# Performance work log

Hardware: AMD Instinct MI355X
Metric: run time of the kernel (lower is better)

The kernel has to match this reference:

```python
import jax, jax.numpy as jnp
import numpy as np
from jax import lax

B, DIM, H, W = 4, 256, 128, 128
KS, LOC, STRIDES_CFG, HEADS = 5, [2, 3], [1, 2], 8
C2 = DIM // 2
GK = HEADS * KS  # per-pixel dynamic kernel channels

def _kernel_map(ks, kstride, kloc):
    # replicates LSAMixer.generate_kernel_map_1d
    axes, strides, start = [0], [1], 1
    for loc, s in zip(kloc, kstride):
        for num in range(0, loc - start):
            axes.append(num * s + axes[-1] + strides[-1])
            strides.append(s)
        start = loc
    patch = (axes[-1] + strides[-1]) * 2 - 1
    full_axes = [-a for a in axes[:0:-1]] + axes
    full_strides = strides[:0:-1] + strides
    return full_axes, full_strides, patch

OFFS, STRDS, PATCH = _kernel_map(KS, STRIDES_CFG, LOC)
PAD = PATCH // 2

def _pw(x, w, b):
    # 1x1 conv as GEMM
    return jnp.einsum('bchw,oc->bohw', x, w) + b[None, :, None, None]

def _dw(x, w, b, ph, pw):
    # depthwise conv, torch OIHW layout with I=1
    y = lax.conv_general_dilated(x, w, (1, 1), [(ph, ph), (pw, pw)],
                                 feature_group_count=x.shape[1],
                                 dimension_numbers=('NCHW', 'OIHW', 'NCHW'))
    return y + b[None, :, None, None]

def _fsa(x, kern, groups, axis):
    # dynamic local attention: for each tap k (offset a, stride s) gather the
    # average of x over the s-wide strided window along `axis`, weight it by
    # the per-head dynamic kernel, and accumulate.
    Bx, Cx, Hx, Wx = x.shape
    gd = Cx // groups
    K = len(OFFS)
    L = x.shape[axis]
    padcfg = [(0, 0)] * 4
    padcfg[axis] = (PAD, PAD)
    xp = jnp.pad(x, padcfg)
    taps = []
    for a, s in zip(OFFS, STRDS):
        start = a if a >= 0 else a - s + 1  # window covers s pixels away from center
        acc = lax.slice_in_dim(xp, PAD + start, PAD + start + L, axis=axis)
        for d in range(1, s):
            acc = acc + lax.slice_in_dim(xp, PAD + start + d, PAD + start + d + L, axis=axis)
        taps.append(acc / s)
    t = jnp.stack(taps, 0).reshape(K, Bx, groups, gd, Hx, Wx)
    k = kern.reshape(Bx, groups, K, Hx, Wx)
    return jnp.einsum('kbgdhw,bgkhw->bgdhw', t, k).reshape(Bx, Cx, Hx, Wx)

def setup_inputs() -> dict:
    key = jax.random.key(0)
    ks = jax.random.split(key, 12)
    sc = 0.02
    f32 = jnp.float32
    return {
        'x': jax.random.normal(ks[0], (B, DIM, H, W), f32),
        'proj_in_w': jax.random.normal(ks[1], (DIM, DIM), f32) * sc,
        'proj_in_b': jnp.zeros((DIM,), f32),
        'hk_dw_w': jax.random.normal(ks[2], (C2, 1, 1, PATCH), f32) * sc,
        'hk_dw_b': jnp.zeros((C2,), f32),
        'hk_pw_w': jax.random.normal(ks[3], (GK, C2), f32) * sc,
        'hk_pw_b': jnp.zeros((GK,), f32),
        'vk_dw_w': jax.random.normal(ks[4], (C2, 1, PATCH, 1), f32) * sc,
        'vk_dw_b': jnp.zeros((C2,), f32),
        'vk_pw_w': jax.random.normal(ks[5], (GK, C2), f32) * sc,
        'vk_pw_b': jnp.zeros((GK,), f32),
        'cb_w1': jax.random.normal(ks[6], (DIM // 4, C2), f32) * sc,
        'cb_b1': jnp.zeros((DIM // 4,), f32),
        'cb_w2': jax.random.normal(ks[7], (C2, DIM // 4), f32) * sc,
        'cb_b2': jnp.zeros((C2,), f32),
        'proj_out_w': jax.random.normal(ks[8], (DIM, DIM), f32) * sc,
        'proj_out_b': jnp.zeros((DIM,), f32),
    }

def reference(x, proj_in_w, proj_in_b, hk_dw_w, hk_dw_b, hk_pw_w, hk_pw_b,
              vk_dw_w, vk_dw_b, vk_pw_w, vk_pw_b, cb_w1, cb_b1, cb_w2, cb_b2,
              proj_out_w, proj_out_b):
    Bv, _, Hv, Wv = x.shape
    h = _pw(x, proj_in_w, proj_in_b)
    x1, x2 = h[:, :C2], h[:, C2:]
    # channel branch: pw -> relu -> pw
    x_conv = _pw(jax.nn.relu(_pw(x1, cb_w1, cb_b1)), cb_w2, cb_b2)
    # horizontal dynamic kernel + fsa
    kh = jnp.tanh(_pw(_dw(x2, hk_dw_w, hk_dw_b, 0, PAD), hk_pw_w, hk_pw_b))
    attn_h = _fsa(x2, kh, HEADS, axis=3)
    # vertical dynamic kernel + fsa
    kv = jnp.tanh(_pw(_dw(attn_h, vk_dw_w, vk_dw_b, PAD, 0), vk_pw_w, vk_pw_b))
    attn = _fsa(attn_h, kv, HEADS, axis=2)
    N = Hv * Wv
    xc = x_conv.reshape(Bv, C2, N)
    at = attn.reshape(Bv, C2, N)
    # SpatialInteraction(x_conv, attn): modulates x_conv
    s_sig = jax.nn.sigmoid(jnp.einsum('bc,bcn->bn', at.mean(-1), xc) / C2)[:, None, :]
    spatial_map = (s_sig * xc).reshape(Bv, C2, Hv, Wv)
    # ChannelInteraction(x_conv, attn): modulates attn
    c_sig = jax.nn.sigmoid(jnp.einsum('bcn,bn->bc', at, xc.mean(1)) / N)[:, :, None]
    channel_map = (c_sig * at).reshape(Bv, C2, Hv, Wv)
    out = jnp.concatenate([spatial_map, channel_map], axis=1)
    return _pw(out, proj_out_w, proj_out_b)
```

## Files before the change

### kernel.cpp

```cpp
#include <hip/hip_runtime.h>
#include <hip/hip_bf16.h>
#include <math.h>

typedef __hip_bfloat16 bf16;
typedef __attribute__((ext_vector_type(8))) short short8;
typedef __attribute__((ext_vector_type(4))) float floatx4;
#define DEV __device__ __forceinline__

constexpr int BATCH = 4;
constexpr int DIM   = 256;
constexpr int C2    = 128;
constexpr int GK    = 40;
constexpr int HH    = 128;
constexpr int WW    = 128;
constexpr int NPIX  = HH * WW;
constexpr int TPB   = 256;

DEV float toF(float v) { return v; }
DEV float toF(bf16 v)  { return __bfloat162float(v); }

DEV unsigned short f2bs(float f) {
  union { bf16 h; unsigned short u; } cv;
  cv.h = __float2bfloat16(f);
  return cv.u;
}
DEV float bs2f(unsigned short u) {
  union { float f; unsigned x; } c;
  c.x = ((unsigned)u) << 16;
  return c.f;
}

template<int N>
DEV void load_f32v(const float* __restrict__ p, float* v) {
  if constexpr (N == 8) {
    const float4 a = *(const float4*)p;
    const float4 b = *(const float4*)(p + 4);
    v[0]=a.x; v[1]=a.y; v[2]=a.z; v[3]=a.w; v[4]=b.x; v[5]=b.y; v[6]=b.z; v[7]=b.w;
  } else if constexpr (N == 4) {
    const float4 a = *(const float4*)p;
    v[0]=a.x; v[1]=a.y; v[2]=a.z; v[3]=a.w;
  } else {
    const float2 a = *(const float2*)p;
    v[0]=a.x; v[1]=a.y;
  }
}
template<int N>
DEV void load_bf16v(const bf16* __restrict__ p, float* v) {
  if constexpr (N == 8) {
    const uint4 u = *(const uint4*)p;
    v[0]=bs2f(u.x & 0xffff); v[1]=bs2f(u.x >> 16);
    v[2]=bs2f(u.y & 0xffff); v[3]=bs2f(u.y >> 16);
    v[4]=bs2f(u.z & 0xffff); v[5]=bs2f(u.z >> 16);
    v[6]=bs2f(u.w & 0xffff); v[7]=bs2f(u.w >> 16);
  } else if constexpr (N == 4) {
    const uint2 u = *(const uint2*)p;
    v[0]=bs2f(u.x & 0xffff); v[1]=bs2f(u.x >> 16);
    v[2]=bs2f(u.y & 0xffff); v[3]=bs2f(u.y >> 16);
  } else {
    const unsigned u = *(const unsigned*)p;
    v[0]=bs2f(u & 0xffff); v[1]=bs2f(u >> 16);
  }
}
DEV void load8bf(const bf16* __restrict__ p, float* v) { load_bf16v<8>(p, v); }

__global__ __launch_bounds__(TPB) void prepack_kernel(
    const float* __restrict__ w0, const float* __restrict__ w1,
    const float* __restrict__ w2, const float* __restrict__ w3,
    const float* __restrict__ w4, const float* __restrict__ w5,
    short* __restrict__ dst) {
  const int i = blockIdx.x * TPB + threadIdx.x;
  if (i >= 157696) return;
  int j = i;
  float v;
  if (j < 65536) v = w0[j];
  else if ((j -= 65536) < 8192) v = w1[j];
  else if ((j -= 8192) < 8192) v = w2[j];
  else if ((j -= 8192) < 5120) v = w3[j];
  else if ((j -= 5120) < 5120) v = w4[j];
  else { j -= 5120; v = w5[j]; }
  dst[i] = (short)f2bs(v);
}

template<int K, int O, int ACT, int GATED, typename TIN, typename TOUT>
__global__ __launch_bounds__(TPB) void pw2_kernel(
    const TIN* __restrict__ in, int in_bs,
    const short* __restrict__ wbf, const float* __restrict__ bias,
    TOUT* __restrict__ out, int out_bs,
    const bf16* __restrict__ gxc, const bf16* __restrict__ gattn,
    const float* __restrict__ gs, const float* __restrict__ gc) {
  constexpr int C8   = K / 8;
  constexpr int PXT  = K / 32;
  constexpr int PG   = 64 / PXT;
  constexpr int ROWB = K * 2 + 16;
  constexpr int WO   = (O + 63) / 64;
  __shared__ char smem[64 * ROWB];

  const int p0   = blockIdx.x * 64;
  const int b    = blockIdx.y;
  const int t    = threadIdx.x;
  const int lane = t & 63, wid = t >> 6;
  const int q    = lane >> 4, i16 = lane & 15;

  {
    const int c8  = t / PG;
    const int px0 = (t % PG) * PXT;
    float vals[8][PXT];
    float svals[PXT];
    if constexpr (GATED) {
      if (c8 < C8 / 2) load_f32v<PXT>(gs + (size_t)b * NPIX + p0 + px0, svals);
    }
#pragma unroll
    for (int j = 0; j < 8; ++j) {
      const int c = c8 * 8 + j;
      float tmp[PXT];
      if constexpr (GATED) {
        if (c < C2) {
          load_bf16v<PXT>(gxc + ((size_t)b * C2 + c) * NPIX + p0 + px0, tmp);
#pragma unroll
          for (int px = 0; px < PXT; ++px) vals[j][px] = tmp[px] * svals[px];
        } else {
          const float cg = gc[b * C2 + (c - C2)];
          load_bf16v<PXT>(gattn + ((size_t)b * C2 + (c - C2)) * NPIX + p0 + px0, tmp);
#pragma unroll
          for (int px = 0; px < PXT; ++px) vals[j][px] = tmp[px] * cg;
        }
      } else {
        const TIN* src = in + ((size_t)b * in_bs + c) * NPIX + p0 + px0;
        if constexpr (sizeof(TIN) == 4) load_f32v<PXT>((const float*)src, tmp);
        else                            load_bf16v<PXT>((const bf16*)src, tmp);
#pragma unroll
        for (int px = 0; px < PXT; ++px) vals[j][px] = tmp[px];
      }
    }
#pragma unroll
    for (int px = 0; px < PXT; ++px) {
      const int p = px0 + px;
      short8 pk;
#pragma unroll
      for (int j = 0; j < 8; ++j) pk[j] = (short)f2bs(vals[j][px]);
      const int phys = c8 ^ ((p >> 3) & 7);
      *reinterpret_cast<short8*>(smem + (size_t)p * ROWB + phys * 16) = pk;
    }
  }
  __syncthreads();

  const int o_base = wid * WO * 16;
  if (o_base >= O) return;

  floatx4 acc[WO][4];
#pragma unroll
  for (int ot = 0; ot < WO; ++ot)
#pragma unroll
    for (int nt = 0; nt < 4; ++nt)
      acc[ot][nt] = (floatx4){0.f, 0.f, 0.f, 0.f};

  for (int kc = 0; kc < K / 32; ++kc) {
    short8 afrag[WO];
#pragma unroll
    for (int ot = 0; ot < WO; ++ot) {
      int o = o_base + ot * 16 + i16;
      if (o >= O) o = O - 1;
      afrag[ot] = *reinterpret_cast<const short8*>(wbf + (size_t)o * K + kc * 32 + q * 8);
    }
    short8 bfrag[4];
#pragma unroll
    for (int nt = 0; nt < 4; ++nt) {
      const int n = nt * 16 + i16;
      const int phys = (kc * 4 + q) ^ ((n >> 3) & 7);
      bfrag[nt] = *reinterpret_cast<const short8*>(smem + (size_t)n * ROWB + phys * 16);
    }
#pragma unroll
    for (int ot = 0; ot < WO; ++ot)
#pragma unroll
      for (int nt = 0; nt < 4; ++nt)
        acc[ot][nt] = __builtin_amdgcn_mfma_f32_16x16x32_bf16(
            afrag[ot], bfrag[nt], acc[ot][nt], 0, 0, 0);
  }

#pragma unroll
  for (int ot = 0; ot < WO; ++ot) {
#pragma unroll
    for (int reg = 0; reg < 4; ++reg) {
      const int o = o_base + ot * 16 + q * 4 + reg;
      if (o < O) {
        const float bv = bias[o];
#pragma unroll
        for (int nt = 0; nt < 4; ++nt) {
          float v = acc[ot][nt][reg] + bv;
          if (ACT == 1) v = fmaxf(v, 0.0f);
          if (ACT == 2) v = tanhf(v);
          TOUT* dst = out + ((size_t)b * out_bs + o) * NPIX + p0 + nt * 16 + i16;
          if constexpr (sizeof(TOUT) == 4) *dst = v;
          else *dst = __float2bfloat16(v);
        }
      }
    }
  }
}

__global__ __launch_bounds__(TPB) void pwfused_kernel(
    const float* __restrict__ x,
    const short* __restrict__ w_pi, const float* __restrict__ pib,
    const short* __restrict__ w_cb1, const float* __restrict__ cbb1,
    const short* __restrict__ w_cb2, const float* __restrict__ cbb2,
    float* __restrict__ x2out, bf16* __restrict__ xconv) {
  constexpr int ROWB  = 256 * 2 + 16;
  constexpr int HROWB = 128 * 2 + 16;
  constexpr int TROWB = 64 * 2 + 16;
  __shared__ char smem[64 * ROWB];
  __shared__ char hbuf[64 * HROWB];
  __shared__ char tbuf[64 * TROWB];

  const int p0   = blockIdx.x * 64;
  const int b    = blockIdx.y;
  const int t    = threadIdx.x;
  const int lane = t & 63, wid = t >> 6;
  const int q    = lane >> 4, i16 = lane & 15;

  {
    const int c8  = t / 8;
    const int px0 = (t % 8) * 8;
    float vals[8][8];
#pragma unroll
    for (int j = 0; j < 8; ++j) {
      const int c = c8 * 8 + j;
      load_f32v<8>(x + ((size_t)b * DIM + c) * NPIX + p0 + px0, vals[j]);
    }
#pragma unroll
    for (int px = 0; px < 8; ++px) {
      const int p = px0 + px;
      short8 pk;
#pragma unroll
      for (int j = 0; j < 8; ++j) pk[j] = (short)f2bs(vals[j][px]);
      const int phys = c8 ^ ((p >> 3) & 7);
      *reinterpret_cast<short8*>(smem + (size_t)p * ROWB + phys * 16) = pk;
    }
  }
  __syncthreads();

  const int o_base = wid * 64;
  {
    floatx4 acc[4][4];
#pragma unroll
    for (int ot = 0; ot < 4; ++ot)
#pragma unroll
      for (int nt = 0; nt < 4; ++nt)
        acc[ot][nt] = (floatx4){0.f, 0.f, 0.f, 0.f};

    for (int kc = 0; kc < 8; ++kc) {
      short8 afrag[4];
#pragma unroll
      for (int ot = 0; ot < 4; ++ot) {
        const int o = o_base + ot * 16 + i16;
        afrag[ot] = *reinterpret_cast<const short8*>(w_pi + (size_t)o * 256 + kc * 32 + q * 8);
      }
      short8 bfrag[4];
#pragma unroll
      for (int nt = 0; nt < 4; ++nt) {
        const int n = nt * 16 + i16;
        const int phys = (kc * 4 + q) ^ ((n >> 3) & 7);
        bfrag[nt] = *reinterpret_cast<const short8*>(smem + (size_t)n * ROWB + phys * 16);
      }
#pragma unroll
      for (int ot = 0; ot < 4; ++ot)
#pragma unroll
        for (int nt = 0; nt < 4; ++nt)
          acc[ot][nt] = __builtin_amdgcn_mfma_f32_16x16x32_bf16(
              afrag[ot], bfrag[nt], acc[ot][nt], 0, 0, 0);
    }

#pragma unroll
    for (int ot = 0; ot < 4; ++ot) {
      const int ch0 = o_base + ot * 16 + q * 4;
      if (ch0 >= C2) {
#pragma unroll
        for (int reg = 0; reg < 4; ++reg) {
          const int o = ch0 + reg;
          const float bv = pib[o];
#pragma unroll
          for (int nt = 0; nt < 4; ++nt)
            x2out[((size_t)b * C2 + (o - C2)) * NPIX + p0 + nt * 16 + i16] =
                acc[ot][nt][reg] + bv;
        }
      } else {
        float bv4[4];
#pragma unroll
        for (int reg = 0; reg < 4; ++reg) bv4[reg] = pib[ch0 + reg];
#pragma unroll
        for (int nt = 0; nt < 4; ++nt) {
          const int px = nt * 16 + i16;
          ushort4 pk;
          pk.x = f2bs(acc[ot][nt][0] + bv4[0]);
          pk.y = f2bs(acc[ot][nt][1] + bv4[1]);
          pk.z = f2bs(acc[ot][nt][2] + bv4[2]);
          pk.w = f2bs(acc[ot][nt][3] + bv4[3]);
          const int phys = (ch0 >> 3) ^ ((px >> 3) & 7);
          *reinterpret_cast<ushort4*>(hbuf + (size_t)px * HROWB + phys * 16 +
                                      (ch0 & 7) * 2) = pk;
        }
      }
    }
  }
  __syncthreads();

  {
    floatx4 acc2[4];
#pragma unroll
    for (int nt = 0; nt < 4; ++nt) acc2[nt] = (floatx4){0.f, 0.f, 0.f, 0.f};
    const int o2b = wid * 16;
    for (int kc = 0; kc < 4; ++kc) {
      const short8 afrag = *reinterpret_cast<const short8*>(
          w_cb1 + (size_t)(o2b + i16) * 128 + kc * 32 + q * 8);
      short8 bfrag[4];
#pragma unroll
      for (int nt = 0; nt < 4; ++nt) {
        const int n = nt * 16 + i16;
        const int phys = (kc * 4 + q) ^ ((n >> 3) & 7);
        bfrag[nt] = *reinterpret_cast<const short8*>(hbuf + (size_t)n * HROWB + phys * 16);
      }
#pragma unroll
      for (int nt = 0; nt < 4; ++nt)
        acc2[nt] = __builtin_amdgcn_mfma_f32_16x16x32_bf16(afrag, bfrag[nt], acc2[nt], 0, 0, 0);
    }
    const int ch0 = o2b + q * 4;
    float bv4[4];
#pragma unroll
    for (int reg = 0; reg < 4; ++reg) bv4[reg] = cbb1[ch0 + reg];
#pragma unroll
    for (int nt = 0; nt < 4; ++nt) {
      const int px = nt * 16 + i16;
      ushort4 pk;
      pk.x = f2bs(fmaxf(acc2[nt][0] + bv4[0], 0.f));
      pk.y = f2bs(fmaxf(acc2[nt][1] + bv4[1], 0.f));
      pk.z = f2bs(fmaxf(acc2[nt][2] + bv4[2], 0.f));
      pk.w = f2bs(fmaxf(acc2[nt][3] + bv4[3], 0.f));
      const int phys = (ch0 >> 3) ^ ((px >> 3) & 7);
      *reinterpret_cast<ushort4*>(tbuf + (size_t)px * TROWB + phys * 16 +
                                  (ch0 & 7) * 2) = pk;
    }
  }
  __syncthreads();

  {
    floatx4 acc3[2][4];
#pragma unroll
    for (int ot = 0; ot < 2; ++ot)
#pragma unroll
      for (int nt = 0; nt < 4; ++nt) acc3[ot][nt] = (floatx4){0.f, 0.f, 0.f, 0.f};
    const int o3b = wid * 32;
    for (int kc = 0; kc < 2; ++kc) {
      short8 afrag[2];
#pragma unroll
      for (int ot = 0; ot < 2; ++ot)
        afrag[ot] = *reinterpret_cast<const short8*>(
            w_cb2 + (size_t)(o3b + ot * 16 + i16) * 64 + kc * 32 + q * 8);
      short8 bfrag[4];
#pragma unroll
      for (int nt = 0; nt < 4; ++nt) {
        const int n = nt * 16 + i16;
        const int phys = (kc * 4 + q) ^ ((n >> 3) & 7);
        bfrag[nt] = *reinterpret_cast<const short8*>(tbuf + (size_t)n * TROWB + phys * 16);
      }
#pragma unroll
      for (int ot = 0; ot < 2; ++ot)
#pragma unroll
        for (int nt = 0; nt < 4; ++nt)
          acc3[ot][nt] = __builtin_amdgcn_mfma_f32_16x16x32_bf16(
              afrag[ot], bfrag[nt], acc3[ot][nt], 0, 0, 0);
    }
#pragma unroll
    for (int ot = 0; ot < 2; ++ot) {
#pragma unroll
      for (int reg = 0; reg < 4; ++reg) {
        const int o = o3b + ot * 16 + q * 4 + reg;
        const float bv = cbb2[o];
#pragma unroll
        for (int nt = 0; nt < 4; ++nt)
          xconv[((size_t)b * C2 + o) * NPIX + p0 + nt * 16 + i16] =
              __float2bfloat16(acc3[ot][nt][reg] + bv);
      }
    }
  }
}

__global__ __launch_bounds__(TPB) void dwh2_kernel(
    const float* __restrict__ in, int in_bs,
    const float* __restrict__ w7, const float* __restrict__ bias,
    bf16* __restrict__ out) {
  const int g  = blockIdx.x * TPB + threadIdx.x;
  const int w8 = g & 15;
  const int hp = (g >> 4) & (HH - 1);
  const int c  = (g >> 11) & (C2 - 1);
  const int b  = g >> 18;
  const float* xr = in + ((size_t)b * in_bs + c) * NPIX + hp * WW;
  const int px0 = w8 * 8;
  float xs[14];
  if (w8 > 0) { const float4 L = *(const float4*)(xr + px0 - 4); xs[0]=L.y; xs[1]=L.z; xs[2]=L.w; }
  else { xs[0]=xs[1]=xs[2]=0.f; }
  { const float4 a = *(const float4*)(xr + px0);
    const float4 bq = *(const float4*)(xr + px0 + 4);
    xs[3]=a.x; xs[4]=a.y; xs[5]=a.z; xs[6]=a.w;
    xs[7]=bq.x; xs[8]=bq.y; xs[9]=bq.z; xs[10]=bq.w; }
  if (w8 < 15) { const float4 R = *(const float4*)(xr + px0 + 8); xs[11]=R.x; xs[12]=R.y; xs[13]=R.z; }
  else { xs[11]=xs[12]=xs[13]=0.f; }
  float wv[7];
#pragma unroll
  for (int j = 0; j < 7; ++j) wv[j] = w7[c * 7 + j];
  const float bv = bias[c];
  short8 o;
#pragma unroll
  for (int i = 0; i < 8; ++i) {
    float a = bv;
#pragma unroll
    for (int j = 0; j < 7; ++j) a = fmaf(wv[j], xs[i + j], a);
    o[i] = (short)f2bs(a);
  }
  *reinterpret_cast<short8*>(out + ((size_t)(b * C2 + c)) * NPIX + hp * WW + px0) = o;
}

__global__ __launch_bounds__(TPB) void dwv2_kernel(
    const bf16* __restrict__ in,
    const float* __restrict__ w7, const float* __restrict__ bias,
    bf16* __restrict__ out) {
  const int g  = blockIdx.x * TPB + threadIdx.x;
  const int w8 = g & 15;
  const int hp = (g >> 4) & (HH - 1);
  const int c  = (g >> 11) & (C2 - 1);
  const int b  = g >> 18;
  const int px0 = w8 * 8;
  const bf16* base = in + ((size_t)(b * C2 + c)) * NPIX + px0;
  float r[7][8];
#pragma unroll
  for (int j = 0; j < 7; ++j) {
    const int hq = hp - 3 + j;
    if (hq >= 0 && hq < HH) load8bf(base + (size_t)hq * WW, r[j]);
    else
#pragma unroll
      for (int i = 0; i < 8; ++i) r[j][i] = 0.f;
  }
  float wv[7];
#pragma unroll
  for (int j = 0; j < 7; ++j) wv[j] = w7[c * 7 + j];
  const float bv = bias[c];
  short8 o;
#pragma unroll
  for (int i = 0; i < 8; ++i) {
    float a = bv;
#pragma unroll
    for (int j = 0; j < 7; ++j) a = fmaf(wv[j], r[j][i], a);
    o[i] = (short)f2bs(a);
  }
  *reinterpret_cast<short8*>(out + ((size_t)(b * C2 + c)) * NPIX + hp * WW + px0) = o;
}

DEV float block_reduce_sum(float v) {
#pragma unroll
  for (int off = 32; off > 0; off >>= 1) v += __shfl_down(v, off, 64);
  __shared__ float ls[TPB / 64];
  const int lane = threadIdx.x & 63;
  const int wid  = threadIdx.x >> 6;
  if (lane == 0) ls[wid] = v;
  __syncthreads();
  float s = 0.0f;
  if (threadIdx.x == 0) {
#pragma unroll
    for (int i = 0; i < TPB / 64; ++i) s += ls[i];
  }
  return s;
}

__global__ __launch_bounds__(TPB) void fsah2_kernel(
    const float* __restrict__ x, int x_bs,
    const bf16* __restrict__ kern, bf16* __restrict__ out) {
  const int g  = blockIdx.x * TPB + threadIdx.x;
  const int w8 = g & 15;
  const int hp = (g >> 4) & (HH - 1);
  const int c  = (g >> 11) & (C2 - 1);
  const int b  = g >> 18;
  const float* xr = x + ((size_t)b * x_bs + c) * NPIX + hp * WW;
  const int px0 = w8 * 8;
  float xs[14];
  if (w8 > 0) { const float4 L = *(const float4*)(xr + px0 - 4); xs[0]=L.y; xs[1]=L.z; xs[2]=L.w; }
  else { xs[0]=xs[1]=xs[2]=0.f; }
  { const float4 a = *(const float4*)(xr + px0);
    const float4 bq = *(const float4*)(xr + px0 + 4);
    xs[3]=a.x; xs[4]=a.y; xs[5]=a.z; xs[6]=a.w;
    xs[7]=bq.x; xs[8]=bq.y; xs[9]=bq.z; xs[10]=bq.w; }
  if (w8 < 15) { const float4 R = *(const float4*)(xr + px0 + 8); xs[11]=R.x; xs[12]=R.y; xs[13]=R.z; }
  else { xs[11]=xs[12]=xs[13]=0.f; }
  float k[5][8];
  const bf16* kr = kern + ((size_t)b * GK + (c >> 4) * 5) * NPIX + hp * WW + px0;
#pragma unroll
  for (int tp = 0; tp < 5; ++tp) load8bf(kr + (size_t)tp * NPIX, k[tp]);
  short8 o;
#pragma unroll
  for (int i = 0; i < 8; ++i) {
    float a = 0.5f * (xs[i] + xs[i + 1]) * k[0][i];
    a = fmaf(xs[i + 2], k[1][i], a);
    a = fmaf(xs[i + 3], k[2][i], a);
    a = fmaf(xs[i + 4], k[3][i], a);
    a = fmaf(0.5f * (xs[i + 5] + xs[i + 6]), k[4][i], a);
    o[i] = (short)f2bs(a);
  }
  *reinterpret_cast<short8*>(out + ((size_t)(b * C2 + c)) * NPIX + hp * WW + px0) = o;
}

__global__ __launch_bounds__(TPB) void fsav2_kernel(
    const bf16* __restrict__ x,
    const bf16* __restrict__ kern, bf16* __restrict__ out,
    float* __restrict__ at_mean) {
  const int g  = blockIdx.x * TPB + threadIdx.x;
  const int w8 = g & 15;
  const int hp = (g >> 4) & (HH - 1);
  const int c  = (g >> 11) & (C2 - 1);
  const int b  = g >> 18;
  const int px0 = w8 * 8;
  const bf16* base = x + ((size_t)(b * C2 + c)) * NPIX + px0;
  float r[7][8];
#pragma unroll
  for (int j = 0; j < 7; ++j) {
    const int hq = hp - 3 + j;
    if (hq >= 0 && hq < HH) load8bf(base + (size_t)hq * WW, r[j]);
    else
#pragma unroll
      for (int i = 0; i < 8; ++i) r[j][i] = 0.f;
  }
  float k[5][8];
  const bf16* kr = kern + ((size_t)b * GK + (c >> 4) * 5) * NPIX + hp * WW + px0;
#pragma unroll
  for (int tp = 0; tp < 5; ++tp) load8bf(kr + (size_t)tp * NPIX, k[tp]);
  short8 o;
  float ps = 0.0f;
#pragma unroll
  for (int i = 0; i < 8; ++i) {
    float a = 0.5f * (r[0][i] + r[1][i]) * k[0][i];
    a = fmaf(r[2][i], k[1][i], a);
    a = fmaf(r[3][i], k[2][i], a);
    a = fmaf(r[4][i], k[3][i], a);
    a = fmaf(0.5f * (r[5][i] + r[6][i]), k[4][i], a);
    o[i] = (short)f2bs(a);
    ps += bs2f((unsigned short)o[i]);
  }
  *reinterpret_cast<short8*>(out + ((size_t)(b * C2 + c)) * NPIX + hp * WW + px0) = o;
  const float s = block_reduce_sum(ps);
  if (threadIdx.x == 0) atomicAdd(&at_mean[b * C2 + c], s);
}

__global__ __launch_bounds__(TPB) void xs_kernel(const bf16* __restrict__ xc,
                                                 const float* __restrict__ at_mean,
                                                 float* __restrict__ xc_mean,
                                                 float* __restrict__ s_sig) {
  __shared__ float am[C2];
  const int b = blockIdx.y;
  if (threadIdx.x < C2) am[threadIdx.x] = at_mean[b * C2 + threadIdx.x] * (1.0f / NPIX);
  __syncthreads();
  const int p = blockIdx.x * TPB + threadIdx.x;
  const bf16* r = xc + (size_t)b * C2 * NPIX + p;
  float s = 0.0f, m = 0.0f;
#pragma unroll 4
  for (int c = 0; c < C2; ++c) {
    const float v = toF(r[(size_t)c * NPIX]);
    m += v;
    s = fmaf(am[c], v, s);
  }
  xc_mean[(size_t)b * NPIX + p] = m * (1.0f / C2);
  s_sig[(size_t)b * NPIX + p]   = 1.0f / (1.0f + expf(-s * (1.0f / C2)));
}

__global__ __launch_bounds__(TPB) void csig_kernel(const bf16* __restrict__ attn,
                                                   const float* __restrict__ xc_mean,
                                                   float* __restrict__ out) {
  const int bc = blockIdx.x;
  const int b  = bc / C2;
  const bf16* r = attn + (size_t)bc * NPIX;
  const float* m = xc_mean + (size_t)b * NPIX;
  float s = 0.0f;
  for (int i = threadIdx.x * 8; i < NPIX; i += TPB * 8) {
    float v[8], mm[8];
    load8bf(r + i, v);
    load_f32v<8>(m + i, mm);
#pragma unroll
    for (int j = 0; j < 8; ++j) s = fmaf(v[j], mm[j], s);
  }
  s = block_reduce_sum(s);
  if (threadIdx.x == 0) out[bc] = 1.0f / (1.0f + expf(-s * (1.0f / NPIX)));
}

extern "C" void kernel_launch(void* const* d_in, const int* in_sizes, int n_in,
                              void* d_out, int out_size, void* d_ws, size_t ws_size,
                              hipStream_t stream) {
  const float* x    = (const float*)d_in[0];
  const float* piw  = (const float*)d_in[1];
  const float* pib  = (const float*)d_in[2];
  const float* hkdw = (const float*)d_in[3];
  const float* hkdb = (const float*)d_in[4];
  const float* hkpw = (const float*)d_in[5];
  const float* hkpb = (const float*)d_in[6];
  const float* vkdw = (const float*)d_in[7];
  const float* vkdb = (const float*)d_in[8];
  const float* vkpw = (const float*)d_in[9];
  const float* vkpb = (const float*)d_in[10];
  const float* cbw1 = (const float*)d_in[11];
  const float* cbb1 = (const float*)d_in[12];
  const float* cbw2 = (const float*)d_in[13];
  const float* cbb2 = (const float*)d_in[14];
  const float* pow_ = (const float*)d_in[15];
  const float* pob  = (const float*)d_in[16];
  float* out = (float*)d_out;

  char* ws = (char*)d_ws;
  size_t off = 0;
  auto alloc = [&](size_t bytes) -> char* {
    char* p = ws + off;
    off += (bytes + 255) & ~(size_t)255;
    return p;
  };
  short* wpk    = (short*)alloc(157696 * 2);
  float* x2buf  = (float*)alloc((size_t)BATCH * C2  * NPIX * 4);
  bf16*  x_conv = (bf16*) alloc((size_t)BATCH * C2  * NPIX * 2);
  bf16*  dwbuf  = (bf16*) alloc((size_t)BATCH * C2  * NPIX * 2);
  bf16*  kbuf   = (bf16*) alloc((size_t)BATCH * GK  * NPIX * 2);
  bf16*  attn_h = (bf16*) alloc((size_t)BATCH * C2  * NPIX * 2);
  bf16*  attn   = (bf16*) alloc((size_t)BATCH * C2  * NPIX * 2);
  float* at_mean = (float*)alloc((size_t)BATCH * C2 * 4);
  float* xc_mean = (float*)alloc((size_t)BATCH * NPIX * 4);
  float* s_sig   = (float*)alloc((size_t)BATCH * NPIX * 4);
  float* c_sig   = (float*)alloc((size_t)BATCH * C2 * 4);

  const short* w_pi  = wpk;
  const short* w_cb1 = wpk + 65536;
  const short* w_cb2 = wpk + 73728;
  const short* w_hk  = wpk + 81920;
  const short* w_vk  = wpk + 87040;
  const short* w_po  = wpk + 92160;

  const dim3 blk(TPB);
  const dim3 gemm_grid(NPIX / 64, BATCH);
  const int PT  = NPIX / TPB;
  const int EL8 = BATCH * C2 * HH * 16 / TPB;

  prepack_kernel<<<dim3((157696 + TPB - 1) / TPB), blk, 0, stream>>>(
      piw, cbw1, cbw2, hkpw, vkpw, pow_, wpk);
  hipMemsetAsync(at_mean, 0, (size_t)BATCH * C2 * 4, stream);
  pwfused_kernel<<<gemm_grid, blk, 0, stream>>>(
      x, w_pi, pib, w_cb1, cbb1, w_cb2, cbb2, x2buf, x_conv);
  dwh2_kernel<<<dim3(EL8), blk, 0, stream>>>(x2buf, C2, hkdw, hkdb, dwbuf);
  pw2_kernel<128, 40, 2, 0, bf16, bf16><<<gemm_grid, blk, 0, stream>>>(
      dwbuf, C2, w_hk, hkpb, kbuf, GK, nullptr, nullptr, nullptr, nullptr);
  fsah2_kernel<<<dim3(EL8), blk, 0, stream>>>(x2buf, C2, kbuf, attn_h);
  dwv2_kernel<<<dim3(EL8), blk, 0, stream>>>(attn_h, vkdw, vkdb, dwbuf);
  pw2_kernel<128, 40, 2, 0, bf16, bf16><<<gemm_grid, blk, 0, stream>>>(
      dwbuf, C2, w_vk, vkpb, kbuf, GK, nullptr, nullptr, nullptr, nullptr);
  fsav2_kernel<<<dim3(EL8), blk, 0, stream>>>(attn_h, kbuf, attn, at_mean);
  xs_kernel<<<dim3(PT, BATCH), blk, 0, stream>>>(x_conv, at_mean, xc_mean, s_sig);
  csig_kernel<<<dim3(BATCH * C2), blk, 0, stream>>>(attn, xc_mean, c_sig);
  pw2_kernel<256, 256, 0, 1, bf16, float><<<gemm_grid, blk, 0, stream>>>(
      x_conv, 0, w_po, pob, out, DIM, x_conv, attn, s_sig, c_sig);
}
```

Measured before the change: 285.3 us.

## Fuse dynamic-kernel pointwise GEMM with tanh into FSA apply kernels

The 128->40 pointwise GEMM plus tanh that produces the dynamic kernels now runs inside the FSA kernels. Each block computes its 40x64 kernel tile with MFMA into shared memory and applies it directly, so the kbuf round trip through global memory and two kernel launches go away. In exchange, the FSA apply uses a different thread mapping (64-pixel tiles across all channels). The vertical pass now issues per-8-thread atomics on at_mean instead of per-block ones, which means many more atomics.

```diff
diff --git a/kernel.cpp b/kernel.cpp
--- a/kernel.cpp
+++ b/kernel.cpp
@@ -453,6 +453,237 @@
   *reinterpret_cast<short8*>(out + ((size_t)(b * C2 + c)) * NPIX + hp * WW + px0) = o;
 }
 
+__global__ __launch_bounds__(TPB) void fsahk_kernel(
+    const bf16* __restrict__ dwin,
+    const float* __restrict__ x2,
+    const short* __restrict__ wpw, const float* __restrict__ pwb,
+    bf16* __restrict__ outp) {
+  constexpr int ROWB = 128 * 2 + 16;
+  constexpr int KROW = 64 * 2 + 16;
+  __shared__ char smem[64 * ROWB];
+  __shared__ char khs[GK * KROW];
+
+  const int p0   = blockIdx.x * 64;
+  const int b    = blockIdx.y;
+  const int t    = threadIdx.x;
+  const int lane = t & 63, wid = t >> 6;
+  const int q    = lane >> 4, i16 = lane & 15;
+
+  {
+    const int c8  = t / 16;
+    const int pxs = (t % 16) * 4;
+    float vals[8][4];
+#pragma unroll
+    for (int j = 0; j < 8; ++j)
+      load_bf16v<4>(dwin + ((size_t)b * C2 + c8 * 8 + j) * NPIX + p0 + pxs, vals[j]);
+#pragma unroll
+    for (int px = 0; px < 4; ++px) {
+      const int p = pxs + px;
+      short8 pk;
+#pragma unroll
+      for (int j = 0; j < 8; ++j) pk[j] = (short)f2bs(vals[j][px]);
+      const int phys = c8 ^ ((p >> 3) & 7);
+      *reinterpret_cast<short8*>(smem + (size_t)p * ROWB + phys * 16) = pk;
+    }
+  }
+  __syncthreads();
+
+  if (wid * 16 < GK) {
+    const int o_base = wid * 16;
+    floatx4 acc[4];
+#pragma unroll
+    for (int nt = 0; nt < 4; ++nt) acc[nt] = (floatx4){0.f, 0.f, 0.f, 0.f};
+    for (int kc = 0; kc < 4; ++kc) {
+      int o = o_base + i16;
+      if (o >= GK) o = GK - 1;
+      const short8 afrag = *reinterpret_cast<const short8*>(
+          wpw + (size_t)o * 128 + kc * 32 + q * 8);
+      short8 bfrag[4];
+#pragma unroll
+      for (int nt = 0; nt < 4; ++nt) {
+        const int n = nt * 16 + i16;
+        const int phys = (kc * 4 + q) ^ ((n >> 3) & 7);
+        bfrag[nt] = *reinterpret_cast<const short8*>(smem + (size_t)n * ROWB + phys * 16);
+      }
+#pragma unroll
+      for (int nt = 0; nt < 4; ++nt)
+        acc[nt] = __builtin_amdgcn_mfma_f32_16x16x32_bf16(afrag, bfrag[nt], acc[nt], 0, 0, 0);
+    }
+#pragma unroll
+    for (int reg = 0; reg < 4; ++reg) {
+      const int o = o_base + q * 4 + reg;
+      if (o < GK) {
+        const float bv = pwb[o];
+#pragma unroll
+        for (int nt = 0; nt < 4; ++nt) {
+          const int px = nt * 16 + i16;
+          *reinterpret_cast<unsigned short*>(khs + (size_t)o * KROW + px * 2) =
+              f2bs(tanhf(acc[nt][reg] + bv));
+        }
+      }
+    }
+  }
+  __syncthreads();
+
+  const int row   = p0 >> 7;
+  const int wbase = p0 & (WW - 1);
+#pragma unroll
+  for (int iter = 0; iter < 4; ++iter) {
+    const int unit = iter * 256 + t;
+    const int c    = unit >> 3;
+    const int pxl  = (unit & 7) * 8;
+    const int wpos = wbase + pxl;
+    const float* xr = x2 + ((size_t)b * C2 + c) * NPIX + row * WW;
+    float xs[14];
+    if (wpos > 0) { const float4 L = *(const float4*)(xr + wpos - 4); xs[0]=L.y; xs[1]=L.z; xs[2]=L.w; }
+    else { xs[0]=xs[1]=xs[2]=0.f; }
+    { const float4 a = *(const float4*)(xr + wpos);
+      const float4 bq = *(const float4*)(xr + wpos + 4);
+      xs[3]=a.x; xs[4]=a.y; xs[5]=a.z; xs[6]=a.w;
+      xs[7]=bq.x; xs[8]=bq.y; xs[9]=bq.z; xs[10]=bq.w; }
+    if (wpos < 120) { const float4 R = *(const float4*)(xr + wpos + 8); xs[11]=R.x; xs[12]=R.y; xs[13]=R.z; }
+    else { xs[11]=xs[12]=xs[13]=0.f; }
+    float k5[5][8];
+    const int gg = c >> 4;
+#pragma unroll
+    for (int tp = 0; tp < 5; ++tp) {
+      const short8 kv = *reinterpret_cast<const short8*>(
+          khs + (size_t)(gg * 5 + tp) * KROW + pxl * 2);
+#pragma unroll
+      for (int i = 0; i < 8; ++i) k5[tp][i] = bs2f((unsigned short)kv[i]);
+    }
+    short8 o8;
+#pragma unroll
+    for (int i = 0; i < 8; ++i) {
+      float a = 0.5f * (xs[i] + xs[i + 1]) * k5[0][i];
+      a = fmaf(xs[i + 2], k5[1][i], a);
+      a = fmaf(xs[i + 3], k5[2][i], a);
+      a = fmaf(xs[i + 4], k5[3][i], a);
+      a = fmaf(0.5f * (xs[i + 5] + xs[i + 6]), k5[4][i], a);
+      o8[i] = (short)f2bs(a);
+    }
+    *reinterpret_cast<short8*>(outp + ((size_t)(b * C2 + c)) * NPIX + p0 + pxl) = o8;
+  }
+}
+
+__global__ __launch_bounds__(TPB) void fsavk_kernel(
+    const bf16* __restrict__ dwin,
+    const bf16* __restrict__ ah,
+    const short* __restrict__ wpw, const float* __restrict__ pwb,
+    bf16* __restrict__ outp, float* __restrict__ at_mean) {
+  constexpr int ROWB = 128 * 2 + 16;
+  constexpr int KROW = 64 * 2 + 16;
+  __shared__ char smem[64 * ROWB];
+  __shared__ char khs[GK * KROW];
+
+  const int p0   = blockIdx.x * 64;
+  const int b    = blockIdx.y;
+  const int t    = threadIdx.x;
+  const int lane = t & 63, wid = t >> 6;
+  const int q    = lane >> 4, i16 = lane & 15;
+
+  {
+    const int c8  = t / 16;
+    const int pxs = (t % 16) * 4;
+    float vals[8][4];
+#pragma unroll
+    for (int j = 0; j < 8; ++j)
+      load_bf16v<4>(dwin + ((size_t)b * C2 + c8 * 8 + j) * NPIX + p0 + pxs, vals[j]);
+#pragma unroll
+    for (int px = 0; px < 4; ++px) {
+      const int p = pxs + px;
+      short8 pk;
+#pragma unroll
+      for (int j = 0; j < 8; ++j) pk[j] = (short)f2bs(vals[j][px]);
+      const int phys = c8 ^ ((p >> 3) & 7);
+      *reinterpret_cast<short8*>(smem + (size_t)p * ROWB + phys * 16) = pk;
+    }
+  }
+  __syncthreads();
+
+  if (wid * 16 < GK) {
+    const int o_base = wid * 16;
+    floatx4 acc[4];
+#pragma unroll
+    for (int nt = 0; nt < 4; ++nt) acc[nt] = (floatx4){0.f, 0.f, 0.f, 0.f};
+    for (int kc = 0; kc < 4; ++kc) {
+      int o = o_base + i16;
+      if (o >= GK) o = GK - 1;
+      const short8 afrag = *reinterpret_cast<const short8*>(
+          wpw + (size_t)o * 128 + kc * 32 + q * 8);
+      short8 bfrag[4];
+#pragma unroll
+      for (int nt = 0; nt < 4; ++nt) {
+        const int n = nt * 16 + i16;
+        const int phys = (kc * 4 + q) ^ ((n >> 3) & 7);
+        bfrag[nt] = *reinterpret_cast<const short8*>(smem + (size_t)n * ROWB + phys * 16);
+      }
+#pragma unroll
+      for (int nt = 0; nt < 4; ++nt)
+        acc[nt] = __builtin_amdgcn_mfma_f32_16x16x32_bf16(afrag, bfrag[nt], acc[nt], 0, 0, 0);
+    }
+#pragma unroll
+    for (int reg = 0; reg < 4; ++reg) {
+      const int o = o_base + q * 4 + reg;
+      if (o < GK) {
+        const float bv = pwb[o];
+#pragma unroll
+        for (int nt = 0; nt < 4; ++nt) {
+          const int px = nt * 16 + i16;
+          *reinterpret_cast<unsigned short*>(khs + (size_t)o * KROW + px * 2) =
+              f2bs(tanhf(acc[nt][reg] + bv));
+        }
+      }
+    }
+  }
+  __syncthreads();
+
+  const int row   = p0 >> 7;
+  const int wbase = p0 & (WW - 1);
+#pragma unroll
+  for (int iter = 0; iter < 4; ++iter) {
+    const int unit = iter * 256 + t;
+    const int c    = unit >> 3;
+    const int pxl  = (unit & 7) * 8;
+    const int wpos = wbase + pxl;
+    const bf16* base = ah + ((size_t)b * C2 + c) * NPIX + wpos;
+    float r[7][8];
+#pragma unroll
+    for (int k = 0; k < 7; ++k) {
+      const int hq = row - 3 + k;
+      if (hq >= 0 && hq < HH) load8bf(base + (size_t)hq * WW, r[k]);
+      else
+#pragma unroll
+        for (int i = 0; i < 8; ++i) r[k][i] = 0.f;
+    }
+    float k5[5][8];
+    const int gg = c >> 4;
+#pragma unroll
+    for (int tp = 0; tp < 5; ++tp) {
+      const short8 kv = *reinterpret_cast<const short8*>(
+          khs + (size_t)(gg * 5 + tp) * KROW + pxl * 2);
+#pragma unroll
+      for (int i = 0; i < 8; ++i) k5[tp][i] = bs2f((unsigned short)kv[i]);
+    }
+    short8 o8;
+    float ps = 0.0f;
+#pragma unroll
+    for (int i = 0; i < 8; ++i) {
+      float a = 0.5f * (r[0][i] + r[1][i]) * k5[0][i];
+      a = fmaf(r[2][i], k5[1][i], a);
+      a = fmaf(r[3][i], k5[2][i], a);
+      a = fmaf(r[4][i], k5[3][i], a);
+      a = fmaf(0.5f * (r[5][i] + r[6][i]), k5[4][i], a);
+      o8[i] = (short)f2bs(a);
+      ps += bs2f((unsigned short)o8[i]);
+    }
+    *reinterpret_cast<short8*>(outp + ((size_t)(b * C2 + c)) * NPIX + p0 + pxl) = o8;
+#pragma unroll
+    for (int off = 4; off > 0; off >>= 1) ps += __shfl_down(ps, off, 8);
+    if ((t & 7) == 0) atomicAdd(&at_mean[b * C2 + c], ps);
+  }
+}
+
 DEV float block_reduce_sum(float v) {
 #pragma unroll
   for (int off = 32; off > 0; off >>= 1) v += __shfl_down(v, off, 64);
@@ -467,83 +698,6 @@
     for (int i = 0; i < TPB / 64; ++i) s += ls[i];
   }
   return s;
-}
-
-__global__ __launch_bounds__(TPB) void fsah2_kernel(
-    const float* __restrict__ x, int x_bs,
-    const bf16* __restrict__ kern, bf16* __restrict__ out) {
-  const int g  = blockIdx.x * TPB + threadIdx.x;
-  const int w8 = g & 15;
-  const int hp = (g >> 4) & (HH - 1);
-  const int c  = (g >> 11) & (C2 - 1);
-  const int b  = g >> 18;
-  const float* xr = x + ((size_t)b * x_bs + c) * NPIX + hp * WW;
-  const int px0 = w8 * 8;
-  float xs[14];
-  if (w8 > 0) { const float4 L = *(const float4*)(xr + px0 - 4); xs[0]=L.y; xs[1]=L.z; xs[2]=L.w; }
-  else { xs[0]=xs[1]=xs[2]=0.f; }
-  { const float4 a = *(const float4*)(xr + px0);
-    const float4 bq = *(const float4*)(xr + px0 + 4);
-    xs[3]=a.x; xs[4]=a.y; xs[5]=a.z; xs[6]=a.w;
-    xs[7]=bq.x; xs[8]=bq.y; xs[9]=bq.z; xs[10]=bq.w; }
-  if (w8 < 15) { const float4 R = *(const float4*)(xr + px0 + 8); xs[11]=R.x; xs[12]=R.y; xs[13]=R.z; }
-  else { xs[11]=xs[12]=xs[13]=0.f; }
-  float k[5][8];
-  const bf16* kr = kern + ((size_t)b * GK + (c >> 4) * 5) * NPIX + hp * WW + px0;
-#pragma unroll
-  for (int tp = 0; tp < 5; ++tp) load8bf(kr + (size_t)tp * NPIX, k[tp]);
-  short8 o;
-#pragma unroll
-  for (int i = 0; i < 8; ++i) {
-    float a = 0.5f * (xs[i] + xs[i + 1]) * k[0][i];
-    a = fmaf(xs[i + 2], k[1][i], a);
-    a = fmaf(xs[i + 3], k[2][i], a);
-    a = fmaf(xs[i + 4], k[3][i], a);
-    a = fmaf(0.5f * (xs[i + 5] + xs[i + 6]), k[4][i], a);
-    o[i] = (short)f2bs(a);
-  }
-  *reinterpret_cast<short8*>(out + ((size_t)(b * C2 + c)) * NPIX + hp * WW + px0) = o;
-}
-
-__global__ __launch_bounds__(TPB) void fsav2_kernel(
-    const bf16* __restrict__ x,
-    const bf16* __restrict__ kern, bf16* __restrict__ out,
-    float* __restrict__ at_mean) {
-  const int g  = blockIdx.x * TPB + threadIdx.x;
-  const int w8 = g & 15;
-  const int hp = (g >> 4) & (HH - 1);
-  const int c  = (g >> 11) & (C2 - 1);
-  const int b  = g >> 18;
-  const int px0 = w8 * 8;
-  const bf16* base = x + ((size_t)(b * C2 + c)) * NPIX + px0;
-  float r[7][8];
-#pragma unroll
-  for (int j = 0; j < 7; ++j) {
-    const int hq = hp - 3 + j;
-    if (hq >= 0 && hq < HH) load8bf(base + (size_t)hq * WW, r[j]);
-    else
-#pragma unroll
-      for (int i = 0; i < 8; ++i) r[j][i] = 0.f;
-  }
-  float k[5][8];
-  const bf16* kr = kern + ((size_t)b * GK + (c >> 4) * 5) * NPIX + hp * WW + px0;
-#pragma unroll
-  for (int tp = 0; tp < 5; ++tp) load8bf(kr + (size_t)tp * NPIX, k[tp]);
-  short8 o;
-  float ps = 0.0f;
-#pragma unroll
-  for (int i = 0; i < 8; ++i) {
-    float a = 0.5f * (r[0][i] + r[1][i]) * k[0][i];
-    a = fmaf(r[2][i], k[1][i], a);
-    a = fmaf(r[3][i], k[2][i], a);
-    a = fmaf(r[4][i], k[3][i], a);
-    a = fmaf(0.5f * (r[5][i] + r[6][i]), k[4][i], a);
-    o[i] = (short)f2bs(a);
-    ps += bs2f((unsigned short)o[i]);
-  }
-  *reinterpret_cast<short8*>(out + ((size_t)(b * C2 + c)) * NPIX + hp * WW + px0) = o;
-  const float s = block_reduce_sum(ps);
-  if (threadIdx.x == 0) atomicAdd(&at_mean[b * C2 + c], s);
 }
 
 __global__ __launch_bounds__(TPB) void xs_kernel(const bf16* __restrict__ xc,
@@ -619,7 +773,6 @@
   float* x2buf  = (float*)alloc((size_t)BATCH * C2  * NPIX * 4);
   bf16*  x_conv = (bf16*) alloc((size_t)BATCH * C2  * NPIX * 2);
   bf16*  dwbuf  = (bf16*) alloc((size_t)BATCH * C2  * NPIX * 2);
-  bf16*  kbuf   = (bf16*) alloc((size_t)BATCH * GK  * NPIX * 2);
   bf16*  attn_h = (bf16*) alloc((size_t)BATCH * C2  * NPIX * 2);
   bf16*  attn   = (bf16*) alloc((size_t)BATCH * C2  * NPIX * 2);
   float* at_mean = (float*)alloc((size_t)BATCH * C2 * 4);
@@ -645,13 +798,11 @@
   pwfused_kernel<<<gemm_grid, blk, 0, stream>>>(
       x, w_pi, pib, w_cb1, cbb1, w_cb2, cbb2, x2buf, x_conv);
   dwh2_kernel<<<dim3(EL8), blk, 0, stream>>>(x2buf, C2, hkdw, hkdb, dwbuf);
-  pw2_kernel<128, 40, 2, 0, bf16, bf16><<<gemm_grid, blk, 0, stream>>>(
-      dwbuf, C2, w_hk, hkpb, kbuf, GK, nullptr, nullptr, nullptr, nullptr);
-  fsah2_kernel<<<dim3(EL8), blk, 0, stream>>>(x2buf, C2, kbuf, attn_h);
+  fsahk_kernel<<<gemm_grid, blk, 0, stream>>>(
+      dwbuf, x2buf, w_hk, hkpb, attn_h);
   dwv2_kernel<<<dim3(EL8), blk, 0, stream>>>(attn_h, vkdw, vkdb, dwbuf);
-  pw2_kernel<128, 40, 2, 0, bf16, bf16><<<gemm_grid, blk, 0, stream>>>(
-      dwbuf, C2, w_vk, vkpb, kbuf, GK, nullptr, nullptr, nullptr, nullptr);
-  fsav2_kernel<<<dim3(EL8), blk, 0, stream>>>(attn_h, kbuf, attn, at_mean);
+  fsavk_kernel<<<gemm_grid, blk, 0, stream>>>(
+      dwbuf, attn_h, w_vk, vkpb, attn, at_mean);
   xs_kernel<<<dim3(PT, BATCH), blk, 0, stream>>>(x_conv, at_mean, xc_mean, s_sig);
   csig_kernel<<<dim3(BATCH * C2), blk, 0, stream>>>(attn, xc_mean, c_sig);
   pw2_kernel<256, 256, 0, 1, bf16, float><<<gemm_grid, blk, 0, stream>>>(
```

New measurement: 289.6 us. Within noise of the previous version (+1.5%).
